# Performance work log

Measured on AMD Instinct MI355X. Metric: run time of the kernel, lower is better.

The kernel has to match this reference:

```python
import jax, jax.numpy as jnp
import numpy as np

B, CH, D, H, W = 8, 64, 32, 64, 64
S = CH // 2  # shrink


def setup_inputs() -> dict:
    key = jax.random.key(0)
    ks = jax.random.split(key, 10)
    sc = 0.05
    x = jax.random.normal(ks[0], (B, CH, D, H, W), jnp.float32)
    Wk = jax.random.normal(ks[1], (S, CH), jnp.float32) * sc
    bk = jax.random.normal(ks[2], (S,), jnp.float32) * sc
    Wq = jax.random.normal(ks[3], (S, CH), jnp.float32) * sc
    bq = jax.random.normal(ks[4], (S,), jnp.float32) * sc
    Wv = jax.random.normal(ks[5], (S, CH), jnp.float32) * sc
    bv = jax.random.normal(ks[6], (S,), jnp.float32) * sc
    Wo = jax.random.normal(ks[7], (CH, S), jnp.float32) * sc
    bo = jax.random.normal(ks[8], (CH,), jnp.float32) * sc
    # original inits atten_factor to 0 (which zeroes the attention branch);
    # use a nonzero value so the attention path is exercised.
    factor = jnp.full((1,), 0.5, jnp.float32)
    return {"x": x, "Wk": Wk, "bk": bk, "Wq": Wq, "bq": bq,
            "Wv": Wv, "bv": bv, "Wo": Wo, "bo": bo, "factor": factor}


def reference(x, Wk, bk, Wq, bq, Wv, bv, Wo, bo, factor):
    b, c, d, h, w = x.shape
    s = Wk.shape[0]

    def proj(Wm, bm):
        # conv3d 1x1 + permute(0,3,4,1,2) fused: [B,C,D,H,W] -> [B,H,W,S,D]
        y = jnp.einsum('oc,bcdhw->bhwod', Wm, x) + bm[None, None, None, :, None]
        return y.reshape(b * h * w, s, d)

    k = proj(Wk, bk)
    q = proj(Wq, bq)
    v = proj(Wv, bv)
    # scores [N, D, D]; softmax over dim=1 (the k-derived axis), matching torch
    scores = jnp.einsum('nsi,nsj->nij', k, q) / jnp.sqrt(jnp.float32(s))
    a = jax.nn.softmax(scores, axis=1)
    o = jnp.einsum('nsd,ndj->nsj', v, a)                    # [N, S, D]
    o = o.reshape(b, h, w, s, d)
    # output conv1x1 back to C channels, layout [B,C,D,H,W]
    o = jnp.einsum('os,bhwsd->bodhw', Wo, o) + bo[None, :, None, None, None]
    y = x + factor[0] * o
    return jnp.mean(y, axis=2)                              # [B, C, H, W]
```

## Files before the change

kernel.cpp:

```cpp
#include <hip/hip_runtime.h>


namespace {
constexpr int kB = 8, kC = 64, kD = 32, kH = 64, kW = 64, kS = 32;
constexpr int kHW = kH * kW;
constexpr int TW = 8, NT = 256;

typedef unsigned short u16t;
typedef unsigned int u32t;
typedef __attribute__((ext_vector_type(8))) short bf16x8;
typedef __attribute__((ext_vector_type(4))) float f32x4;
typedef __attribute__((ext_vector_type(4))) short short4v;

__device__ __forceinline__ float b2f(u16t u) {
    union { u32t i; float f; } v; v.i = ((u32t)u) << 16; return v.f;
}
__device__ __forceinline__ u16t f2b(float f) {
    union { u32t i; float f; } v; v.f = f;
    u32t r = v.i + 0x7FFFu + ((v.i >> 16) & 1u);
    return (u16t)(r >> 16);
}
__device__ __forceinline__ u32t pack2(float lo, float hi) {
    return (u32t)f2b(lo) | ((u32t)f2b(hi) << 16);
}
__device__ __forceinline__ bf16x8 pack8(const float4 f0, const float4 f1) {
    bf16x8 a;
    a[0] = (short)f2b(f0.x); a[1] = (short)f2b(f0.y);
    a[2] = (short)f2b(f0.z); a[3] = (short)f2b(f0.w);
    a[4] = (short)f2b(f1.x); a[5] = (short)f2b(f1.y);
    a[6] = (short)f2b(f1.z); a[7] = (short)f2b(f1.w);
    return a;
}
}

__global__ __launch_bounds__(NT, 4) void attn_fused(
    const float* __restrict__ x,
    const float* __restrict__ Wk, const float* __restrict__ bk,
    const float* __restrict__ Wq, const float* __restrict__ bq,
    const float* __restrict__ Wv, const float* __restrict__ bv,
    const float* __restrict__ Wo, const float* __restrict__ bo,
    const float* __restrict__ factor,
    float* __restrict__ out)
{
    __shared__ __align__(16) u16t KQX[256 * 64];
    __shared__ float XbarS[TW * kC];
    __shared__ float AbarS[TW * kD];
    __shared__ __align__(16) float ObarS[TW * kS];

    const int t = threadIdx.x;
    const int lane = t & 63;
    const int wv = t >> 6;
    const int l15 = lane & 15;
    const int quad = lane >> 4;

    const int blk = blockIdx.x;
    const int bh = (blk & 7) | ((blk >> 6) << 3);
    const int wt = (blk >> 3) & 7;
    const int b = bh >> 6, h = bh & 63, w0 = wt * TW;

    {
        const float* xb = x + (size_t)(b * kC * kD) * kHW + h * kW + w0;
        const int w4 = t & 1, cp = (t >> 1) & 31;
        const float* p0 = xb + (size_t)((cp * 2) * kD + wv) * kHW + w4 * 4;
        const float* p1 = p0 + (size_t)kD * kHW;
        float4 fa[8], fb[8];
        #pragma unroll
        for (int it = 0; it < 8; ++it) {
            fa[it] = *(const float4*)(p0 + (size_t)(it * 4) * kHW);
            fb[it] = *(const float4*)(p1 + (size_t)(it * 4) * kHW);
        }
        u32t* dst = (u32t*)KQX;
        const int gsw = cp >> 2;
        const int gin = cp & 3;
        #pragma unroll
        for (int it = 0; it < 8; ++it) {
            int d = wv + it * 4;
            int sw = d & 7;
            int pg = (gsw ^ sw) * 4 + gin;
            int r0 = w4 * 128 + d;
            dst[(r0 + 0 * 32) * 32 + pg] = pack2(fa[it].x, fb[it].x);
            dst[(r0 + 1 * 32) * 32 + pg] = pack2(fa[it].y, fb[it].y);
            dst[(r0 + 2 * 32) * 32 + pg] = pack2(fa[it].z, fb[it].z);
            dst[(r0 + 3 * 32) * 32 + pg] = pack2(fa[it].w, fb[it].w);
        }
    }
    __syncthreads();

    bf16x8 Bf[4][2];
    #pragma unroll
    for (int nt = 0; nt < 4; ++nt) {
        int row = wv * 64 + nt * 16 + l15;
        int sw = l15 & 7;
        #pragma unroll
        for (int ks = 0; ks < 2; ++ks)
            Bf[nt][ks] = *(const bf16x8*)&KQX[row * 64 + ((ks * 4 + quad) ^ sw) * 8];
    }

    #pragma unroll
    for (int hh = 0; hh < 2; ++hh) {
        float xb16[16];
        #pragma unroll
        for (int ks = 0; ks < 2; ++ks)
            #pragma unroll
            for (int e = 0; e < 8; ++e)
                xb16[ks * 8 + e] = b2f((u16t)Bf[hh * 2 + 0][ks][e])
                                 + b2f((u16t)Bf[hh * 2 + 1][ks][e]);
        #pragma unroll
        for (int i = 0; i < 16; ++i) {
            float v = xb16[i];
            v += __shfl_xor(v, 1);
            v += __shfl_xor(v, 2);
            v += __shfl_xor(v, 4);
            v += __shfl_xor(v, 8);
            xb16[i] = v;
        }
        if (l15 == 0) {
            int wp = 2 * wv + hh;
            #pragma unroll
            for (int ks = 0; ks < 2; ++ks)
                #pragma unroll
                for (int e = 0; e < 8; ++e)
                    XbarS[wp * kC + ks * 32 + quad * 8 + e] = xb16[ks * 8 + e] * (1.0f / kD);
        }
    }

    short4v Vp[2][4];
    #pragma unroll
    for (int p = 0; p < 3; ++p) {
        const float* Wp = (p == 0) ? Wk : (p == 1) ? Wq : Wv;
        const float* bp = (p == 0) ? bk : (p == 1) ? bq : bv;
        bf16x8 Af[2][2];
        float4 bias4[2];
        #pragma unroll
        for (int m0 = 0; m0 < 2; ++m0) {
            #pragma unroll
            for (int ks = 0; ks < 2; ++ks) {
                const float* src = Wp + (m0 * 16 + l15) * kC + ks * 32 + quad * 8;
                Af[m0][ks] = pack8(*(const float4*)src, *(const float4*)(src + 4));
            }
            bias4[m0] = *(const float4*)(bp + m0 * 16 + quad * 4);
        }
        #pragma unroll
        for (int m0 = 0; m0 < 2; ++m0) {
            #pragma unroll
            for (int nt = 0; nt < 4; ++nt) {
                f32x4 acc = {0.f, 0.f, 0.f, 0.f};
                acc = __builtin_amdgcn_mfma_f32_16x16x32_bf16(Af[m0][0], Bf[nt][0], acc, 0, 0, 0);
                acc = __builtin_amdgcn_mfma_f32_16x16x32_bf16(Af[m0][1], Bf[nt][1], acc, 0, 0, 0);
                short4v pk;
                pk.x = (short)f2b(acc[0] + bias4[m0].x);
                pk.y = (short)f2b(acc[1] + bias4[m0].y);
                pk.z = (short)f2b(acc[2] + bias4[m0].z);
                pk.w = (short)f2b(acc[3] + bias4[m0].w);
                if (p < 2) {
                    int row = wv * 64 + nt * 16 + l15;
                    int g = (p == 0 ? 0 : 4) + m0 * 2 + (quad >> 1);
                    *(short4v*)&KQX[row * 64 + ((g ^ (l15 & 7)) * 8) + (quad & 1) * 4] = pk;
                } else {
                    Vp[m0][nt] = pk;
                }
            }
        }
    }

    {
        const float kScaleLog2e = 0.25501700249569946f;
        #pragma unroll
        for (int si = 0; si < 2; ++si) {
            int wp = wv * 2 + si;
            bf16x8 Ka[2], Qb[2];
            #pragma unroll
            for (int m0 = 0; m0 < 2; ++m0) {
                int rr = wp * 32 + m0 * 16 + l15;
                Ka[m0] = *(const bf16x8*)&KQX[rr * 64 + ((quad ^ (l15 & 7)) * 8)];
            }
            #pragma unroll
            for (int n0 = 0; n0 < 2; ++n0) {
                int rr = wp * 32 + n0 * 16 + l15;
                Qb[n0] = *(const bf16x8*)&KQX[rr * 64 + (((4 + quad) ^ (l15 & 7)) * 8)];
            }
            f32x4 sc[2][2];
            #pragma unroll
            for (int m0 = 0; m0 < 2; ++m0)
                #pragma unroll
                for (int n0 = 0; n0 < 2; ++n0) {
                    f32x4 z = {0.f, 0.f, 0.f, 0.f};
                    sc[m0][n0] = __builtin_amdgcn_mfma_f32_16x16x32_bf16(Ka[m0], Qb[n0], z, 0, 0, 0);
                }
            #pragma unroll
            for (int n0 = 0; n0 < 2; ++n0) {
                float sum = 0.f;
                #pragma unroll
                for (int m0 = 0; m0 < 2; ++m0)
                    #pragma unroll
                    for (int r2 = 0; r2 < 4; ++r2) {
                        float e = exp2f(sc[m0][n0][r2] * kScaleLog2e);
                        sc[m0][n0][r2] = e; sum += e;
                    }
                sum += __shfl_xor(sum, 16);
                sum += __shfl_xor(sum, 32);
                float inv = __builtin_amdgcn_rcpf(sum);
                #pragma unroll
                for (int m0 = 0; m0 < 2; ++m0)
                    #pragma unroll
                    for (int r2 = 0; r2 < 4; ++r2) sc[m0][n0][r2] *= inv;
            }
            #pragma unroll
            for (int m0 = 0; m0 < 2; ++m0)
                #pragma unroll
                for (int r2 = 0; r2 < 4; ++r2) {
                    float v2 = sc[m0][0][r2] + sc[m0][1][r2];
                    v2 += __shfl_xor(v2, 1);
                    v2 += __shfl_xor(v2, 2);
                    v2 += __shfl_xor(v2, 4);
                    v2 += __shfl_xor(v2, 8);
                    if (l15 == 0)
                        AbarS[wp * kD + m0 * 16 + quad * 4 + r2] = v2 * (1.0f / kD);
                }
            {
                float ab0 = AbarS[wp * kD + l15];
                float ab1 = AbarS[wp * kD + 16 + l15];
                #pragma unroll
                for (int m0 = 0; m0 < 2; ++m0)
                    #pragma unroll
                    for (int r2 = 0; r2 < 4; ++r2) {
                        float v = b2f((u16t)Vp[m0][2 * si + 0][r2]) * ab0
                                + b2f((u16t)Vp[m0][2 * si + 1][r2]) * ab1;
                        v += __shfl_xor(v, 1);
                        v += __shfl_xor(v, 2);
                        v += __shfl_xor(v, 4);
                        v += __shfl_xor(v, 8);
                        if (l15 == 0)
                            ObarS[wp * kS + m0 * 16 + quad * 4 + r2] = v;
                    }
            }
        }
    }
    __syncthreads();

    {
        const float fac = factor[0];
        int wp = t & 7, cl = t >> 3;
        const float4* obp = (const float4*)&ObarS[wp * kS];
        float4 ob4[8];
        #pragma unroll
        for (int s4 = 0; s4 < 8; ++s4) ob4[s4] = obp[s4];
        #pragma unroll
        for (int half = 0; half < 2; ++half) {
            int c = cl + half * 32;
            const float4* wrow = (const float4*)(Wo + c * kS);
            float acc = 0.f;
            #pragma unroll
            for (int s4 = 0; s4 < 8; ++s4) {
                float4 w4 = wrow[s4];
                acc += w4.x * ob4[s4].x;
                acc += w4.y * ob4[s4].y;
                acc += w4.z * ob4[s4].z;
                acc += w4.w * ob4[s4].w;
            }
            out[((b * kC + c) * kH + h) * kW + w0 + wp] =
                XbarS[wp * kC + c] + fac * (bo[c] + acc);
        }
    }
}

extern "C" void kernel_launch(void* const* d_in, const int* in_sizes, int n_in,
                              void* d_out, int out_size, void* d_ws, size_t ws_size,
                              hipStream_t stream) {
    const float* x      = (const float*)d_in[0];
    const float* Wk     = (const float*)d_in[1];
    const float* bk     = (const float*)d_in[2];
    const float* Wq     = (const float*)d_in[3];
    const float* bq     = (const float*)d_in[4];
    const float* Wv     = (const float*)d_in[5];
    const float* bv     = (const float*)d_in[6];
    const float* Wo     = (const float*)d_in[7];
    const float* bo     = (const float*)d_in[8];
    const float* factor = (const float*)d_in[9];
    float* out = (float*)d_out;

    dim3 grid(kB * kH * (kW / TW));
    attn_fused<<<grid, NT, 0, stream>>>(x, Wk, bk, Wq, bq, Wv, bv, Wo, bo, factor, out);
}
```

Baseline: 427.9 us.

## Compute x depth-mean from registers, hoist weight loads, use hardware bf16 pack

The depth mean of x is now summed directly from the loaded float4 registers and stored as packed partial sums in shared memory. This replaces the shuffle-based reduction over the bf16 MFMA operands. Projection weights and biases for all three projections are loaded before the barrier so their latency overlaps with the x staging. bf16 conversion uses the hardware packed-convert builtin when available, V is kept in fp32, and ObarS is padded. The cost is higher register pressure from holding all weight fragments and fp32 V, which could reduce occupancy under the 4-block launch bound.

Result: no change. 421.1 us (-1.6%).

```diff
diff --git a/kernel.cpp b/kernel.cpp
--- a/kernel.cpp
+++ b/kernel.cpp
@@ -10,26 +10,37 @@
 typedef unsigned int u32t;
 typedef __attribute__((ext_vector_type(8))) short bf16x8;
 typedef __attribute__((ext_vector_type(4))) float f32x4;
-typedef __attribute__((ext_vector_type(4))) short short4v;
-
-__device__ __forceinline__ float b2f(u16t u) {
-    union { u32t i; float f; } v; v.i = ((u32t)u) << 16; return v.f;
-}
-__device__ __forceinline__ u16t f2b(float f) {
-    union { u32t i; float f; } v; v.f = f;
-    u32t r = v.i + 0x7FFFu + ((v.i >> 16) & 1u);
-    return (u16t)(r >> 16);
-}
+
+#if defined(__has_builtin)
+#if __has_builtin(__builtin_amdgcn_cvt_pk_bf16_f32)
+#define HAS_CVT_PK_BF16 1
+#endif
+#endif
+
 __device__ __forceinline__ u32t pack2(float lo, float hi) {
-    return (u32t)f2b(lo) | ((u32t)f2b(hi) << 16);
+#ifdef HAS_CVT_PK_BF16
+    typedef __attribute__((ext_vector_type(2))) __bf16 v2bf;
+    union { v2bf v; u32t u; } cv;
+    cv.v = __builtin_amdgcn_cvt_pk_bf16_f32(lo, hi);
+    return cv.u;
+#else
+    union { u32t i; float f; } a, b;
+    a.f = lo; b.f = hi;
+    u32t ra = a.i + 0x7FFFu + ((a.i >> 16) & 1u);
+    u32t rb = b.i + 0x7FFFu + ((b.i >> 16) & 1u);
+    return (ra >> 16) | (rb & 0xFFFF0000u);
+#endif
 }
 __device__ __forceinline__ bf16x8 pack8(const float4 f0, const float4 f1) {
-    bf16x8 a;
-    a[0] = (short)f2b(f0.x); a[1] = (short)f2b(f0.y);
-    a[2] = (short)f2b(f0.z); a[3] = (short)f2b(f0.w);
-    a[4] = (short)f2b(f1.x); a[5] = (short)f2b(f1.y);
-    a[6] = (short)f2b(f1.z); a[7] = (short)f2b(f1.w);
-    return a;
+    union { bf16x8 v; u32t u[4]; } r;
+    r.u[0] = pack2(f0.x, f0.y); r.u[1] = pack2(f0.z, f0.w);
+    r.u[2] = pack2(f1.x, f1.y); r.u[3] = pack2(f1.z, f1.w);
+    return r.v;
+}
+__device__ __forceinline__ float bsel(u32t q, int odd) {
+    union { u32t i; float f; } v;
+    v.i = odd ? (q & 0xFFFF0000u) : (q << 16);
+    return v.f;
 }
 }
 
@@ -43,9 +54,9 @@
     float* __restrict__ out)
 {
     __shared__ __align__(16) u16t KQX[256 * 64];
-    __shared__ float XbarS[TW * kC];
+    __shared__ u32t XbP[4 * 256];
     __shared__ float AbarS[TW * kD];
-    __shared__ __align__(16) float ObarS[TW * kS];
+    __shared__ __align__(16) float ObarS[TW * 36];
 
     const int t = threadIdx.x;
     const int lane = t & 63;
@@ -69,9 +80,21 @@
             fa[it] = *(const float4*)(p0 + (size_t)(it * 4) * kHW);
             fb[it] = *(const float4*)(p1 + (size_t)(it * 4) * kHW);
         }
+        __builtin_amdgcn_sched_barrier(0);
+
+        float4 sA = fa[0], sB = fb[0];
+        #pragma unroll
+        for (int it = 1; it < 8; ++it) {
+            sA.x += fa[it].x; sA.y += fa[it].y; sA.z += fa[it].z; sA.w += fa[it].w;
+            sB.x += fb[it].x; sB.y += fb[it].y; sB.z += fb[it].z; sB.w += fb[it].w;
+        }
+        XbP[wv * 256 + w4 * 128 + 0 * 32 + cp] = pack2(sA.x, sB.x);
+        XbP[wv * 256 + w4 * 128 + 1 * 32 + cp] = pack2(sA.y, sB.y);
+        XbP[wv * 256 + w4 * 128 + 2 * 32 + cp] = pack2(sA.z, sB.z);
+        XbP[wv * 256 + w4 * 128 + 3 * 32 + cp] = pack2(sA.w, sB.w);
+
         u32t* dst = (u32t*)KQX;
-        const int gsw = cp >> 2;
-        const int gin = cp & 3;
+        const int gsw = cp >> 2, gin = cp & 3;
         #pragma unroll
         for (int it = 0; it < 8; ++it) {
             int d = wv + it * 4;
@@ -84,6 +107,25 @@
             dst[(r0 + 3 * 32) * 32 + pg] = pack2(fa[it].w, fb[it].w);
         }
     }
+
+    bf16x8 Af[3][2][2];
+    float4 bias4[3][2];
+    {
+        const float* Wp[3] = {Wk, Wq, Wv};
+        const float* bp[3] = {bk, bq, bv};
+        #pragma unroll
+        for (int p = 0; p < 3; ++p) {
+            #pragma unroll
+            for (int m0 = 0; m0 < 2; ++m0) {
+                #pragma unroll
+                for (int ks = 0; ks < 2; ++ks) {
+                    const float* src = Wp[p] + (m0 * 16 + l15) * kC + ks * 32 + quad * 8;
+                    Af[p][m0][ks] = pack8(*(const float4*)src, *(const float4*)(src + 4));
+                }
+                bias4[p][m0] = *(const float4*)(bp[p] + m0 * 16 + quad * 4);
+            }
+        }
+    }
     __syncthreads();
 
     bf16x8 Bf[4][2];
@@ -96,68 +138,28 @@
             Bf[nt][ks] = *(const bf16x8*)&KQX[row * 64 + ((ks * 4 + quad) ^ sw) * 8];
     }
 
-    #pragma unroll
-    for (int hh = 0; hh < 2; ++hh) {
-        float xb16[16];
-        #pragma unroll
-        for (int ks = 0; ks < 2; ++ks)
-            #pragma unroll
-            for (int e = 0; e < 8; ++e)
-                xb16[ks * 8 + e] = b2f((u16t)Bf[hh * 2 + 0][ks][e])
-                                 + b2f((u16t)Bf[hh * 2 + 1][ks][e]);
-        #pragma unroll
-        for (int i = 0; i < 16; ++i) {
-            float v = xb16[i];
-            v += __shfl_xor(v, 1);
-            v += __shfl_xor(v, 2);
-            v += __shfl_xor(v, 4);
-            v += __shfl_xor(v, 8);
-            xb16[i] = v;
-        }
-        if (l15 == 0) {
-            int wp = 2 * wv + hh;
-            #pragma unroll
-            for (int ks = 0; ks < 2; ++ks)
-                #pragma unroll
-                for (int e = 0; e < 8; ++e)
-                    XbarS[wp * kC + ks * 32 + quad * 8 + e] = xb16[ks * 8 + e] * (1.0f / kD);
-        }
-    }
-
-    short4v Vp[2][4];
+    f32x4 Vf[2][4];
     #pragma unroll
     for (int p = 0; p < 3; ++p) {
-        const float* Wp = (p == 0) ? Wk : (p == 1) ? Wq : Wv;
-        const float* bp = (p == 0) ? bk : (p == 1) ? bq : bv;
-        bf16x8 Af[2][2];
-        float4 bias4[2];
-        #pragma unroll
-        for (int m0 = 0; m0 < 2; ++m0) {
-            #pragma unroll
-            for (int ks = 0; ks < 2; ++ks) {
-                const float* src = Wp + (m0 * 16 + l15) * kC + ks * 32 + quad * 8;
-                Af[m0][ks] = pack8(*(const float4*)src, *(const float4*)(src + 4));
-            }
-            bias4[m0] = *(const float4*)(bp + m0 * 16 + quad * 4);
-        }
         #pragma unroll
         for (int m0 = 0; m0 < 2; ++m0) {
             #pragma unroll
             for (int nt = 0; nt < 4; ++nt) {
                 f32x4 acc = {0.f, 0.f, 0.f, 0.f};
-                acc = __builtin_amdgcn_mfma_f32_16x16x32_bf16(Af[m0][0], Bf[nt][0], acc, 0, 0, 0);
-                acc = __builtin_amdgcn_mfma_f32_16x16x32_bf16(Af[m0][1], Bf[nt][1], acc, 0, 0, 0);
-                short4v pk;
-                pk.x = (short)f2b(acc[0] + bias4[m0].x);
-                pk.y = (short)f2b(acc[1] + bias4[m0].y);
-                pk.z = (short)f2b(acc[2] + bias4[m0].z);
-                pk.w = (short)f2b(acc[3] + bias4[m0].w);
+                acc = __builtin_amdgcn_mfma_f32_16x16x32_bf16(Af[p][m0][0], Bf[nt][0], acc, 0, 0, 0);
+                acc = __builtin_amdgcn_mfma_f32_16x16x32_bf16(Af[p][m0][1], Bf[nt][1], acc, 0, 0, 0);
                 if (p < 2) {
+                    u32t lo = pack2(acc[0] + bias4[p][m0].x, acc[1] + bias4[p][m0].y);
+                    u32t hi = pack2(acc[2] + bias4[p][m0].z, acc[3] + bias4[p][m0].w);
                     int row = wv * 64 + nt * 16 + l15;
                     int g = (p == 0 ? 0 : 4) + m0 * 2 + (quad >> 1);
-                    *(short4v*)&KQX[row * 64 + ((g ^ (l15 & 7)) * 8) + (quad & 1) * 4] = pk;
+                    uint2 pr; pr.x = lo; pr.y = hi;
+                    *(uint2*)&KQX[row * 64 + ((g ^ (l15 & 7)) * 8) + (quad & 1) * 4] = pr;
                 } else {
-                    Vp[m0][nt] = pk;
+                    Vf[m0][nt][0] = acc[0] + bias4[2][m0].x;
+                    Vf[m0][nt][1] = acc[1] + bias4[2][m0].y;
+                    Vf[m0][nt][2] = acc[2] + bias4[2][m0].z;
+                    Vf[m0][nt][3] = acc[3] + bias4[2][m0].w;
                 }
             }
         }
@@ -224,14 +226,14 @@
                 for (int m0 = 0; m0 < 2; ++m0)
                     #pragma unroll
                     for (int r2 = 0; r2 < 4; ++r2) {
-                        float v = b2f((u16t)Vp[m0][2 * si + 0][r2]) * ab0
-                                + b2f((u16t)Vp[m0][2 * si + 1][r2]) * ab1;
+                        float v = Vf[m0][2 * si + 0][r2] * ab0
+                                + Vf[m0][2 * si + 1][r2] * ab1;
                         v += __shfl_xor(v, 1);
                         v += __shfl_xor(v, 2);
                         v += __shfl_xor(v, 4);
                         v += __shfl_xor(v, 8);
                         if (l15 == 0)
-                            ObarS[wp * kS + m0 * 16 + quad * 4 + r2] = v;
+                            ObarS[wp * 36 + m0 * 16 + quad * 4 + r2] = v;
                     }
             }
         }
@@ -240,14 +242,22 @@
 
     {
         const float fac = factor[0];
-        int wp = t & 7, cl = t >> 3;
-        const float4* obp = (const float4*)&ObarS[wp * kS];
+        const int wp = t & 7, cl = t >> 3;
+        const float4* obp = (const float4*)&ObarS[wp * 36];
         float4 ob4[8];
         #pragma unroll
         for (int s4 = 0; s4 < 8; ++s4) ob4[s4] = obp[s4];
+        const int xidx = (wp >> 2) * 128 + (wp & 3) * 32;
+        const int odd = cl & 1;
         #pragma unroll
         for (int half = 0; half < 2; ++half) {
             int c = cl + half * 32;
+            int cpi = (cl >> 1) + half * 16;
+            float xbar = bsel(XbP[0 * 256 + xidx + cpi], odd)
+                       + bsel(XbP[1 * 256 + xidx + cpi], odd)
+                       + bsel(XbP[2 * 256 + xidx + cpi], odd)
+                       + bsel(XbP[3 * 256 + xidx + cpi], odd);
+            xbar *= (1.0f / kD);
             const float4* wrow = (const float4*)(Wo + c * kS);
             float acc = 0.f;
             #pragma unroll
@@ -259,7 +269,7 @@
                 acc += w4.w * ob4[s4].w;
             }
             out[((b * kC + c) * kH + h) * kW + w0 + wp] =
-                XbarS[wp * kC + c] + fac * (bo[c] + acc);
+                xbar + fac * (bo[c] + acc);
         }
     }
 }
```
